# Optimization experiments

Hardware: AMD Instinct MI355X
Metric: run time of the kernel (lower is better)

The kernel has to match this reference:

```python
import jax, jax.numpy as jnp
from jax import lax
import numpy as np

B, T, H, C = 64, 512, 1024, 21


def setup_inputs() -> dict:
    key = jax.random.key(0)
    k1, k2, k3, k4 = jax.random.split(key, 4)
    return {
        "sequence_output": jax.random.normal(k1, (B, T, H), dtype=jnp.float32),
        "input_mask": jax.random.randint(k2, (B, T), 0, 2, dtype=jnp.int32),
        "W": jax.random.normal(k3, (H, C), dtype=jnp.float32) * 0.02,
        "b": jnp.zeros((C,), dtype=jnp.float32),
        "transitions": jax.random.normal(k4, (C, C), dtype=jnp.float32) * 0.1,
    }


def crf_decode(logits, transitions, seq_len):
    """Viterbi decode matching tfa.text.crf_decode semantics (length-masked)."""
    Bb, Tt, Cc = logits.shape
    ident = jnp.arange(Cc, dtype=jnp.int32)[None, :]  # identity backpointers

    def fwd_step(state, inp):
        logit_t, t = inp  # [B,C], scalar step index
        scores = state[:, :, None] + transitions[None, :, :]  # [B, C_prev, C_cur]
        bp = jnp.argmax(scores, axis=1).astype(jnp.int32)      # [B, C]
        new_state = jnp.max(scores, axis=1) + logit_t          # [B, C]
        valid = (t < seq_len)[:, None]                          # [B, 1]
        state = jnp.where(valid, new_state, state)
        bp = jnp.where(valid, bp, ident)
        return state, bp

    ts = jnp.arange(1, Tt)
    xs = (jnp.transpose(logits[:, 1:], (1, 0, 2)), ts)
    final_state, bps = lax.scan(fwd_step, logits[:, 0], xs)  # bps: [T-1, B, C]
    last_tag = jnp.argmax(final_state, axis=-1).astype(jnp.int32)  # [B]

    def back_step(tag, bp_t):
        tag = jnp.take_along_axis(bp_t, tag[:, None], axis=1)[:, 0]
        return tag, tag

    _, tags_rev = lax.scan(back_step, last_tag, bps, reverse=True)  # [T-1, B]
    tags = jnp.concatenate([tags_rev, last_tag[None, :]], axis=0)   # [T, B]
    return jnp.transpose(tags, (1, 0))  # [B, T]


def reference(sequence_output, input_mask, W, b, transitions):
    # classifier logits
    logits = jnp.einsum("bth,hc->btc", sequence_output, W) + b  # [B,T,C]
    mask = (input_mask == 1).astype(jnp.int32)
    seq_len = jnp.sum(mask, axis=-1)  # [B]
    decode_tags = crf_decode(logits, transitions, seq_len)
    return jax.nn.one_hot(decode_tags, logits.shape[-1], dtype=jnp.float32), logits
```

## Files before the change

### kernel.cpp

```cpp
#include <hip/hip_runtime.h>
#include <stdint.h>

#define BB 64
#define TT 512
#define HH 1024
#define CC 21

#define GAS __attribute__((address_space(1)))
#define LAS __attribute__((address_space(3)))
__device__ __forceinline__ void gll16(const void* g, void* l) {
    __builtin_amdgcn_global_load_lds((const GAS uint32_t*)g, (LAS uint32_t*)l, 16, 0, 0);
}

#define RL(x, lane) __uint_as_float(__builtin_amdgcn_readlane(__float_as_uint(x), (lane)))

__global__ __launch_bounds__(256) void logits_kernel(
    const float* __restrict__ seq,
    const float* __restrict__ W,
    const float* __restrict__ bias,
    float* __restrict__ logits)
{
    __shared__ __align__(16) float4 xsh[4][3][256];
    __shared__ __align__(16) float  wsh[4][2][16*24];

    const int t = threadIdx.x;
    const int w = t >> 6;
    const int l = t & 63;
    const int row0 = blockIdx.x * 64;
    const int hbase = w * 256;
    const float* seqrow = seq + (size_t)(row0 + l) * HH + hbase;

    float acc[CC];
#pragma unroll
    for (int c = 0; c < CC; ++c) acc[c] = 0.f;

    float wr[6];

    auto issueX = [&](int ch) {
        float4* dst = xsh[w][ch % 3];
#pragma unroll
        for (int it = 0; it < 4; ++it)
            gll16(seqrow + ch * 16 + it * 4, dst + it * 64);
    };
    auto issueW = [&](int ch) {
        const float* wg = W + (size_t)(hbase + ch * 16) * CC;
#pragma unroll
        for (int i = 0; i < 6; ++i) {
            int j = i * 64 + l;
            wr[i] = (j < 16 * CC) ? wg[j] : 0.f;
        }
    };
    auto commitW = [&](int ch) {
        float* wb = wsh[w][ch & 1];
#pragma unroll
        for (int i = 0; i < 6; ++i) {
            int j = i * 64 + l;
            if (j < 16 * CC) wb[(j / CC) * 24 + (j % CC)] = wr[i];
        }
    };
    auto compute = [&](int ch) {
        const float4* xb = xsh[w][ch % 3];
        const float*  wb = wsh[w][ch & 1];
        float4 xq[4];
#pragma unroll
        for (int q = 0; q < 4; ++q) xq[q] = xb[q * 64 + l];
#pragma unroll
        for (int q = 0; q < 4; ++q) {
#pragma unroll
            for (int j = 0; j < 4; ++j) {
                const float4* wrow = (const float4*)(wb + (q * 4 + j) * 24);
                float xc = (&xq[q].x)[j];
#pragma unroll
                for (int r5 = 0; r5 < 6; ++r5) {
                    float4 w4 = wrow[r5];
                    int c0 = r5 * 4;
                    acc[c0] += xc * w4.x;
                    if (c0 + 1 < CC) acc[c0 + 1] += xc * w4.y;
                    if (c0 + 2 < CC) acc[c0 + 2] += xc * w4.z;
                    if (c0 + 3 < CC) acc[c0 + 3] += xc * w4.w;
                }
            }
        }
    };

    issueX(0);
    issueW(0);
    issueX(1);
    asm volatile("s_waitcnt vmcnt(4)" ::: "memory");
    commitW(0);

#pragma unroll 1
    for (int ch = 0; ch < 14; ++ch) {
        issueW(ch + 1);
        issueX(ch + 2);
        compute(ch);
        asm volatile("s_waitcnt vmcnt(4)" ::: "memory");
        commitW(ch + 1);
    }
    issueW(15);
    compute(14);
    asm volatile("s_waitcnt vmcnt(0)" ::: "memory");
    commitW(15);
    compute(15);

    __syncthreads();
    float* comb = (float*)&xsh[0][0][0];
    if (w > 0) {
        float* cr = comb + ((w - 1) * 64 + l) * 22;
#pragma unroll
        for (int c = 0; c < CC; ++c) cr[c] = acc[c];
    }
    __syncthreads();
    if (w == 0) {
        const float* p0 = comb + (size_t)l * 22;
        const float* p1 = comb + (size_t)(64 + l) * 22;
        const float* p2 = comb + (size_t)(128 + l) * 22;
        float* orow = logits + (size_t)(row0 + l) * CC;
#pragma unroll
        for (int c = 0; c < CC; ++c)
            orow[c] = acc[c] + p0[c] + p1[c] + p2[c] + bias[c];
    }
}

__global__ __launch_bounds__(256) void viterbi_kernel(
    const float* __restrict__ logits,
    const int* __restrict__ mask,
    const float* __restrict__ trans,
    float* __restrict__ onehot)
{
    __shared__ __align__(16) float lg[(TT + 1) * CC];
    __shared__ float stS[TT * CC];
    __shared__ float trL[CC * CC];
    __shared__ unsigned char bp[TT * CC];
    __shared__ unsigned char tagl[TT];
    __shared__ unsigned char mapl[12 * CC];
    __shared__ unsigned char bnd[13];

    const int tid = threadIdx.x;
    const int w = tid >> 6;
    const int l = tid & 63;
    const int b = blockIdx.x;

    const float* lb = logits + (size_t)b * TT * CC;
    for (int i = w; i < 42; i += 4)
        gll16(lb + (size_t)(i * 64 + l) * 4, &lg[i * 256]);

    for (int j = tid; j < CC * CC; j += 256) trL[j] = trans[j];

    int sl = 0;
#pragma unroll
    for (int k = 0; k < 8; ++k) sl += mask[b * TT + k * 64 + l];
#pragma unroll
    for (int o = 32; o > 0; o >>= 1) sl += __shfl_xor(sl, o);
    const int idstart = (sl >= 1) ? (sl - 1) : 0;

    asm volatile("s_waitcnt vmcnt(0)" ::: "memory");
    __syncthreads();

    if (w == 0) {
        const bool act = (l < CC);
        const int cc = act ? l : 0;
        float tcol[CC];
#pragma unroll
        for (int cp = 0; cp < CC; ++cp) tcol[cp] = trL[cp * CC + cc];

        float st = lg[cc];
        if (act) stS[l] = st;
        float lgt_next = lg[CC + cc];

#pragma unroll 1
        for (int t = 1; t < sl; ++t) {
            float lgt = lgt_next;
            lgt_next = lg[(t + 1) * CC + cc];
            float sc[CC];
#pragma unroll
            for (int cp = 0; cp < CC; ++cp) sc[cp] = RL(st, cp) + tcol[cp];
            float m0 = fmaxf(fmaxf(sc[0], sc[1]), sc[2]);
            float m1 = fmaxf(fmaxf(sc[3], sc[4]), sc[5]);
            float m2 = fmaxf(fmaxf(sc[6], sc[7]), sc[8]);
            float m3 = fmaxf(fmaxf(sc[9], sc[10]), sc[11]);
            float m4 = fmaxf(fmaxf(sc[12], sc[13]), sc[14]);
            float m5 = fmaxf(fmaxf(sc[15], sc[16]), sc[17]);
            float m6 = fmaxf(fmaxf(sc[18], sc[19]), sc[20]);
            float n0 = fmaxf(fmaxf(m0, m1), m2);
            float n1 = fmaxf(fmaxf(m3, m4), m5);
            float best = fmaxf(fmaxf(n0, n1), m6);
            st = best + lgt;
            if (act) stS[t * CC + l] = st;
        }

        float fs[CC];
#pragma unroll
        for (int cp = 0; cp < CC; ++cp) fs[cp] = RL(st, cp);
        float q0 = fmaxf(fmaxf(fs[0], fs[1]), fs[2]);
        float q1 = fmaxf(fmaxf(fs[3], fs[4]), fs[5]);
        float q2 = fmaxf(fmaxf(fs[6], fs[7]), fs[8]);
        float q3 = fmaxf(fmaxf(fs[9], fs[10]), fs[11]);
        float q4 = fmaxf(fmaxf(fs[12], fs[13]), fs[14]);
        float q5 = fmaxf(fmaxf(fs[15], fs[16]), fs[17]);
        float q6 = fmaxf(fmaxf(fs[18], fs[19]), fs[20]);
        float fbest = fmaxf(fmaxf(fmaxf(q0, q1), fmaxf(q2, q3)),
                            fmaxf(fmaxf(q4, q5), q6));
        int e[CC];
#pragma unroll
        for (int cp = 0; cp < CC; ++cp) e[cp] = (fs[cp] == fbest) ? cp : 63;
        int i0 = min(min(e[0], e[1]), e[2]);
        int i1 = min(min(e[3], e[4]), e[5]);
        int i2 = min(min(e[6], e[7]), e[8]);
        int i3 = min(min(e[9], e[10]), e[11]);
        int i4 = min(min(e[12], e[13]), e[14]);
        int i5 = min(min(e[15], e[16]), e[17]);
        int i6 = min(min(e[18], e[19]), e[20]);
        int last = min(min(min(i0, i1), min(i2, i3)), min(min(i4, i5), i6));
        if (l == 0) tagl[TT - 1] = (unsigned char)last;
    } else {
        int s = (w - 1) * 64 + l;
        if (s < 189) {
            int c0 = s % CC, prow = s / CC;
#pragma unroll 1
            for (int p = idstart + prow; p < TT; p += 9)
                bp[p * CC + c0] = (unsigned char)c0;
        }
    }
    __syncthreads();

    if (tid < 252) {
        const int c0 = tid % CC, tg = tid / CC;
        float tc[CC];
#pragma unroll
        for (int cp = 0; cp < CC; ++cp) tc[cp] = trL[cp * CC + c0];
#pragma unroll 1
        for (int t = 1 + tg; t < sl; t += 12) {
            const float* sp = stS + (t - 1) * CC;
            float bv = sp[0] + tc[0];
            int bi = 0;
#pragma unroll
            for (int cp = 1; cp < CC; ++cp) {
                float v = sp[cp] + tc[cp];
                bool g = v > bv;
                bv = g ? v : bv;
                bi = g ? cp : bi;
            }
            bp[(t - 1) * CC + c0] = (unsigned char)bi;
        }
    }
    __syncthreads();

    if (tid < 252) {
        int g = tid / CC, cand = tid % CC;
        int endp = g * 43;
        int startp = min(g * 43 + 42, TT - 2);
        int m = cand;
#pragma unroll 1
        for (int i = 0; i < 43; ++i) {
            int p = startp - i;
            int pr = (p >= endp) ? p : endp;
            int m2 = bp[pr * CC + m];
            m = (p >= endp) ? m2 : m;
        }
        mapl[g * CC + cand] = (unsigned char)m;
    }
    __syncthreads();

    if (tid == 0) {
        int eb = tagl[TT - 1];
        bnd[12] = (unsigned char)eb;
        for (int g = 11; g >= 0; --g) {
            eb = mapl[g * CC + eb];
            bnd[g] = (unsigned char)eb;
        }
    }
    __syncthreads();

    if (tid < 12) {
        int g = tid;
        int endp = g * 43;
        int startp = min(g * 43 + 42, TT - 2);
        int eb = bnd[g + 1];
#pragma unroll 1
        for (int p = startp; p >= endp; --p) {
            eb = bp[p * CC + eb];
            tagl[p] = (unsigned char)eb;
        }
    }
    __syncthreads();

    if (tid < 252) {
        const int c0 = tid % CC, prow = tid / CC;
        float* ob = onehot + (size_t)b * TT * CC;
#pragma unroll 1
        for (int p = prow; p < TT; p += 12)
            ob[(size_t)p * CC + c0] = (c0 == (int)tagl[p]) ? 1.f : 0.f;
    }
}

extern "C" void kernel_launch(void* const* d_in, const int* in_sizes, int n_in,
                              void* d_out, int out_size, void* d_ws, size_t ws_size,
                              hipStream_t stream) {
    const float* seq   = (const float*)d_in[0];
    const int*   msk   = (const int*)d_in[1];
    const float* W     = (const float*)d_in[2];
    const float* bias  = (const float*)d_in[3];
    const float* trans = (const float*)d_in[4];

    float* onehot_out = (float*)d_out;
    float* logits_out = onehot_out + (size_t)BB * TT * CC;

    logits_kernel<<<512, 256, 0, stream>>>(seq, W, bias, logits_out);
    viterbi_kernel<<<BB, 256, 0, stream>>>(logits_out, msk, trans, onehot_out);
}
```

Baseline: 131.3 us.

## Simplify logits GEMV to direct register loads with 8 waves per block

Replaces the LDS-staged, triple-buffered global_load_lds pipeline in the logits kernel with direct float4 loads of the activations and uniform (scalar-cacheable) loads of W. The hidden dimension is split across 8 waves instead of 4, with a 7-way LDS reduction at the end. The aim is to cut LDS traffic and waitcnt stalls and to raise memory-level parallelism. The Viterbi forward loop also gains a two-step logit prefetch and an early exit for inactive lanes. The risk is that W loads go through the scalar or L1 path, and that the larger block could lower occupancy or register headroom.

```diff
diff --git a/kernel.cpp b/kernel.cpp
--- a/kernel.cpp
+++ b/kernel.cpp
@@ -14,111 +14,60 @@
 
 #define RL(x, lane) __uint_as_float(__builtin_amdgcn_readlane(__float_as_uint(x), (lane)))
 
-__global__ __launch_bounds__(256) void logits_kernel(
+__global__ __launch_bounds__(512) void logits_kernel(
     const float* __restrict__ seq,
     const float* __restrict__ W,
     const float* __restrict__ bias,
     float* __restrict__ logits)
 {
-    __shared__ __align__(16) float4 xsh[4][3][256];
-    __shared__ __align__(16) float  wsh[4][2][16*24];
+    __shared__ float comb[7][64][25];
 
     const int t = threadIdx.x;
-    const int w = t >> 6;
+    const int w = __builtin_amdgcn_readfirstlane(t >> 6);
     const int l = t & 63;
     const int row0 = blockIdx.x * 64;
-    const int hbase = w * 256;
-    const float* seqrow = seq + (size_t)(row0 + l) * HH + hbase;
+    const float* xrow  = seq + (size_t)(row0 + l) * HH + w * 128;
+    const float* wbase = W + (size_t)w * 128 * CC;
 
     float acc[CC];
 #pragma unroll
     for (int c = 0; c < CC; ++c) acc[c] = 0.f;
 
-    float wr[6];
-
-    auto issueX = [&](int ch) {
-        float4* dst = xsh[w][ch % 3];
-#pragma unroll
-        for (int it = 0; it < 4; ++it)
-            gll16(seqrow + ch * 16 + it * 4, dst + it * 64);
-    };
-    auto issueW = [&](int ch) {
-        const float* wg = W + (size_t)(hbase + ch * 16) * CC;
-#pragma unroll
-        for (int i = 0; i < 6; ++i) {
-            int j = i * 64 + l;
-            wr[i] = (j < 16 * CC) ? wg[j] : 0.f;
-        }
-    };
-    auto commitW = [&](int ch) {
-        float* wb = wsh[w][ch & 1];
-#pragma unroll
-        for (int i = 0; i < 6; ++i) {
-            int j = i * 64 + l;
-            if (j < 16 * CC) wb[(j / CC) * 24 + (j % CC)] = wr[i];
-        }
-    };
-    auto compute = [&](int ch) {
-        const float4* xb = xsh[w][ch % 3];
-        const float*  wb = wsh[w][ch & 1];
-        float4 xq[4];
-#pragma unroll
-        for (int q = 0; q < 4; ++q) xq[q] = xb[q * 64 + l];
-#pragma unroll
-        for (int q = 0; q < 4; ++q) {
-#pragma unroll
-            for (int j = 0; j < 4; ++j) {
-                const float4* wrow = (const float4*)(wb + (q * 4 + j) * 24);
-                float xc = (&xq[q].x)[j];
-#pragma unroll
-                for (int r5 = 0; r5 < 6; ++r5) {
-                    float4 w4 = wrow[r5];
-                    int c0 = r5 * 4;
-                    acc[c0] += xc * w4.x;
-                    if (c0 + 1 < CC) acc[c0 + 1] += xc * w4.y;
-                    if (c0 + 2 < CC) acc[c0 + 2] += xc * w4.z;
-                    if (c0 + 3 < CC) acc[c0 + 3] += xc * w4.w;
-                }
-            }
-        }
-    };
-
-    issueX(0);
-    issueW(0);
-    issueX(1);
-    asm volatile("s_waitcnt vmcnt(4)" ::: "memory");
-    commitW(0);
-
-#pragma unroll 1
-    for (int ch = 0; ch < 14; ++ch) {
-        issueW(ch + 1);
-        issueX(ch + 2);
-        compute(ch);
-        asm volatile("s_waitcnt vmcnt(4)" ::: "memory");
-        commitW(ch + 1);
-    }
-    issueW(15);
-    compute(14);
-    asm volatile("s_waitcnt vmcnt(0)" ::: "memory");
-    commitW(15);
-    compute(15);
-
-    __syncthreads();
-    float* comb = (float*)&xsh[0][0][0];
+    float4 xb0 = *(const float4*)(xrow);
+    float4 xb1 = *(const float4*)(xrow + 4);
+
+#pragma unroll 2
+    for (int s = 0; s < 32; ++s) {
+        float4 xv = (s & 1) ? xb1 : xb0;
+        if (s + 2 < 32) {
+            float4 nv = *(const float4*)(xrow + (s + 2) * 4);
+            if (s & 1) xb1 = nv; else xb0 = nv;
+        }
+        const float* wp = wbase + s * 84;
+#pragma unroll
+        for (int j = 0; j < 4; ++j) {
+            float xc = (&xv.x)[j];
+#pragma unroll
+            for (int c = 0; c < CC; ++c)
+                acc[c] += xc * wp[j * CC + c];
+        }
+    }
+
     if (w > 0) {
-        float* cr = comb + ((w - 1) * 64 + l) * 22;
+        float* cr = &comb[w - 1][l][0];
 #pragma unroll
         for (int c = 0; c < CC; ++c) cr[c] = acc[c];
     }
     __syncthreads();
     if (w == 0) {
-        const float* p0 = comb + (size_t)l * 22;
-        const float* p1 = comb + (size_t)(64 + l) * 22;
-        const float* p2 = comb + (size_t)(128 + l) * 22;
         float* orow = logits + (size_t)(row0 + l) * CC;
 #pragma unroll
-        for (int c = 0; c < CC; ++c)
-            orow[c] = acc[c] + p0[c] + p1[c] + p2[c] + bias[c];
+        for (int c = 0; c < CC; ++c) {
+            float s = acc[c] + bias[c];
+#pragma unroll
+            for (int i = 0; i < 7; ++i) s += comb[i][l][c];
+            orow[c] = s;
+        }
     }
 }
 
@@ -128,7 +77,7 @@
     const float* __restrict__ trans,
     float* __restrict__ onehot)
 {
-    __shared__ __align__(16) float lg[(TT + 1) * CC];
+    __shared__ __align__(16) float lg[(TT + 2) * CC];
     __shared__ float stS[TT * CC];
     __shared__ float trL[CC * CC];
     __shared__ unsigned char bp[TT * CC];
@@ -159,60 +108,67 @@
 
     if (w == 0) {
         const bool act = (l < CC);
-        const int cc = act ? l : 0;
-        float tcol[CC];
-#pragma unroll
-        for (int cp = 0; cp < CC; ++cp) tcol[cp] = trL[cp * CC + cc];
-
-        float st = lg[cc];
-        if (act) stS[l] = st;
-        float lgt_next = lg[CC + cc];
-
-#pragma unroll 1
-        for (int t = 1; t < sl; ++t) {
-            float lgt = lgt_next;
-            lgt_next = lg[(t + 1) * CC + cc];
-            float sc[CC];
-#pragma unroll
-            for (int cp = 0; cp < CC; ++cp) sc[cp] = RL(st, cp) + tcol[cp];
-            float m0 = fmaxf(fmaxf(sc[0], sc[1]), sc[2]);
-            float m1 = fmaxf(fmaxf(sc[3], sc[4]), sc[5]);
-            float m2 = fmaxf(fmaxf(sc[6], sc[7]), sc[8]);
-            float m3 = fmaxf(fmaxf(sc[9], sc[10]), sc[11]);
-            float m4 = fmaxf(fmaxf(sc[12], sc[13]), sc[14]);
-            float m5 = fmaxf(fmaxf(sc[15], sc[16]), sc[17]);
-            float m6 = fmaxf(fmaxf(sc[18], sc[19]), sc[20]);
-            float n0 = fmaxf(fmaxf(m0, m1), m2);
-            float n1 = fmaxf(fmaxf(m3, m4), m5);
-            float best = fmaxf(fmaxf(n0, n1), m6);
-            st = best + lgt;
-            if (act) stS[t * CC + l] = st;
-        }
-
-        float fs[CC];
-#pragma unroll
-        for (int cp = 0; cp < CC; ++cp) fs[cp] = RL(st, cp);
-        float q0 = fmaxf(fmaxf(fs[0], fs[1]), fs[2]);
-        float q1 = fmaxf(fmaxf(fs[3], fs[4]), fs[5]);
-        float q2 = fmaxf(fmaxf(fs[6], fs[7]), fs[8]);
-        float q3 = fmaxf(fmaxf(fs[9], fs[10]), fs[11]);
-        float q4 = fmaxf(fmaxf(fs[12], fs[13]), fs[14]);
-        float q5 = fmaxf(fmaxf(fs[15], fs[16]), fs[17]);
-        float q6 = fmaxf(fmaxf(fs[18], fs[19]), fs[20]);
-        float fbest = fmaxf(fmaxf(fmaxf(q0, q1), fmaxf(q2, q3)),
-                            fmaxf(fmaxf(q4, q5), q6));
-        int e[CC];
-#pragma unroll
-        for (int cp = 0; cp < CC; ++cp) e[cp] = (fs[cp] == fbest) ? cp : 63;
-        int i0 = min(min(e[0], e[1]), e[2]);
-        int i1 = min(min(e[3], e[4]), e[5]);
-        int i2 = min(min(e[6], e[7]), e[8]);
-        int i3 = min(min(e[9], e[10]), e[11]);
-        int i4 = min(min(e[12], e[13]), e[14]);
-        int i5 = min(min(e[15], e[16]), e[17]);
-        int i6 = min(min(e[18], e[19]), e[20]);
-        int last = min(min(min(i0, i1), min(i2, i3)), min(min(i4, i5), i6));
-        if (l == 0) tagl[TT - 1] = (unsigned char)last;
+        if (act) {
+            const int cc = l;
+            float tcol[CC];
+#pragma unroll
+            for (int cp = 0; cp < CC; ++cp) tcol[cp] = trL[cp * CC + cc];
+
+            float st = lg[cc];
+            stS[l] = st;
+            int lgo = CC + cc;
+            float lg1 = lg[lgo];
+            float lg2 = lg[lgo + CC];
+            int sto = CC + l;
+
+#pragma unroll 1
+            for (int t = 1; t < sl; ++t) {
+                float sc[CC];
+#pragma unroll
+                for (int cp = 0; cp < CC; ++cp) sc[cp] = RL(st, cp) + tcol[cp];
+                float m0 = fmaxf(fmaxf(sc[0], sc[1]), sc[2]);
+                float m1 = fmaxf(fmaxf(sc[3], sc[4]), sc[5]);
+                float m2 = fmaxf(fmaxf(sc[6], sc[7]), sc[8]);
+                float m3 = fmaxf(fmaxf(sc[9], sc[10]), sc[11]);
+                float m4 = fmaxf(fmaxf(sc[12], sc[13]), sc[14]);
+                float m5 = fmaxf(fmaxf(sc[15], sc[16]), sc[17]);
+                float m6 = fmaxf(fmaxf(sc[18], sc[19]), sc[20]);
+                float n0 = fmaxf(fmaxf(m0, m1), m2);
+                float n1 = fmaxf(fmaxf(m3, m4), m5);
+                float best = fmaxf(fmaxf(n0, n1), m6);
+                st = best + lg1;
+                lg1 = lg2;
+                lg2 = lg[lgo + 2 * CC];
+                lgo += CC;
+                stS[sto] = st;
+                sto += CC;
+            }
+
+            float fs[CC];
+#pragma unroll
+            for (int cp = 0; cp < CC; ++cp) fs[cp] = RL(st, cp);
+            float q0 = fmaxf(fmaxf(fs[0], fs[1]), fs[2]);
+            float q1 = fmaxf(fmaxf(fs[3], fs[4]), fs[5]);
+            float q2 = fmaxf(fmaxf(fs[6], fs[7]), fs[8]);
+            float q3 = fmaxf(fmaxf(fs[9], fs[10]), fs[11]);
+            float q4 = fmaxf(fmaxf(fs[12], fs[13]), fs[14]);
+            float q5 = fmaxf(fmaxf(fs[15], fs[16]), fs[17]);
+            float q6 = fmaxf(fmaxf(fs[18], fs[19]), fs[20]);
+            float fbest = fmaxf(fmaxf(fmaxf(q0, q1), fmaxf(q2, q3)),
+                                fmaxf(fmaxf(q4, q5), q6));
+            int e[CC];
+#pragma unroll
+            for (int cp = 0; cp < CC; ++cp) e[cp] = (fs[cp] == fbest) ? cp : 63;
+            int i0 = min(min(e[0], e[1]), e[2]);
+            int i1 = min(min(e[3], e[4]), e[5]);
+            int i2 = min(min(e[6], e[7]), e[8]);
+            int i3 = min(min(e[9], e[10]), e[11]);
+            int i4 = min(min(e[12], e[13]), e[14]);
+            int i5 = min(min(e[15], e[16]), e[17]);
+            int i6 = min(min(e[18], e[19]), e[20]);
+            int last = min(min(min(i0, i1), min(i2, i3)), min(min(i4, i5), i6));
+            if (l == 0) tagl[TT - 1] = (unsigned char)last;
+        }
     } else {
         int s = (w - 1) * 64 + l;
         if (s < 189) {
@@ -306,6 +262,6 @@
     float* onehot_out = (float*)d_out;
     float* logits_out = onehot_out + (size_t)BB * TT * CC;
 
-    logits_kernel<<<512, 256, 0, stream>>>(seq, W, bias, logits_out);
+    logits_kernel<<<512, 512, 0, stream>>>(seq, W, bias, logits_out);
     viterbi_kernel<<<BB, 256, 0, stream>>>(logits_out, msk, trans, onehot_out);
 }
```

New measurement: 146.2 us. 11.3% more time.
